# Kernel optimization log

Hardware: AMD Instinct MI355X
Metric: run time of the kernel (lower is better)

Reference implementation:

```python
import jax, jax.numpy as jnp
import numpy as np
import math

B, L, D, H = 4, 2048, 1024, 16
HD = D // H


def setup_inputs() -> dict:
    key = jax.random.key(0)
    k1, k2, k3 = jax.random.split(key, 3)
    x = jax.random.normal(k1, (B, L, D), dtype=jnp.float32)
    # Linear weights stored as [in, out] so y = x @ W (equivalent to torch x @ W.T)
    Wqkv = jax.random.normal(k2, (D, 3 * D), dtype=jnp.float32) * (1.0 / math.sqrt(D))
    Wproj = jax.random.normal(k3, (D, D), dtype=jnp.float32) * (1.0 / math.sqrt(D))
    attn_mask = jnp.tril(jnp.ones((L, L), dtype=bool))  # True = attend (causal)
    key_padding_mask = jnp.zeros((B, L), dtype=bool)     # True = padded (none here)
    return {"x": x, "Wqkv": Wqkv, "Wproj": Wproj,
            "attn_mask": attn_mask, "key_padding_mask": key_padding_mask}


def reference(x, Wqkv, Wproj, attn_mask, key_padding_mask):
    Bx, Lx, Dx = x.shape
    qkv = x @ Wqkv                              # [B, L, 3D]
    q, k, v = jnp.split(qkv, 3, axis=-1)
    def shape(t):
        return t.reshape(Bx, Lx, H, HD).transpose(0, 2, 1, 3)  # [B, H, L, hd]
    q, k, v = shape(q), shape(k), shape(v)
    att = jnp.einsum('bhqd,bhkd->bhqk', q, k) / math.sqrt(HD)  # [B, H, L, L]
    neg_inf = jnp.float32(-jnp.inf)
    att = jnp.where(attn_mask[None, None, :, :], att, neg_inf)
    att = jnp.where(key_padding_mask[:, None, None, :], neg_inf, att)
    att = jax.nn.softmax(att, axis=-1)
    y = jnp.einsum('bhqk,bhkd->bhqd', att, v)   # [B, H, L, hd]
    y = y.transpose(0, 2, 1, 3).reshape(Bx, Lx, Dx)
    return y @ Wproj
```

## Files before the change

kernel.cpp:

```cpp
#include <hip/hip_runtime.h>
#include <cstdint>
#include <cstddef>


typedef __attribute__((ext_vector_type(8))) __bf16 bf16x8;
typedef __attribute__((ext_vector_type(4))) __bf16 bf16x4;
typedef __attribute__((ext_vector_type(4))) float f32x4;
typedef __attribute__((ext_vector_type(16))) float f32x16;

__device__ __forceinline__ f32x4 mfma_bf16(bf16x8 a, bf16x8 b, f32x4 c) {
  return __builtin_amdgcn_mfma_f32_16x16x32_bf16(a, b, c, 0, 0, 0);
}

__device__ __forceinline__ f32x16 mfma32(bf16x8 a, bf16x8 b, f32x16 c) {
  return __builtin_amdgcn_mfma_f32_32x32x16_bf16(a, b, c, 0, 0, 0);
}

__device__ __forceinline__ unsigned cvtpk(float a, float b) {
  unsigned r;
  asm("v_cvt_pk_bf16_f32 %0, %1, %2" : "=v"(r) : "v"(a), "v"(b));
  return r;
}

__device__ __forceinline__ void async_copy16(const void* gsrc, void* ldsdst) {
  __builtin_amdgcn_global_load_lds(
      (const __attribute__((address_space(1))) void*)gsrc,
      (__attribute__((address_space(3))) void*)ldsdst, 16, 0, 0);
}

__global__ __launch_bounds__(256) void f32_to_bf16(
    const float* __restrict__ in, __bf16* __restrict__ out) {
  const size_t i = ((size_t)blockIdx.x * 256 + threadIdx.x) * 4;
  const float4 v = *(const float4*)&in[i];
  bf16x4 o = {(__bf16)v.x, (__bf16)v.y, (__bf16)v.z, (__bf16)v.w};
  *(bf16x4*)&out[i] = o;
}

__global__ __launch_bounds__(256) void transpose_f32_bf16(
    const float* __restrict__ in, __bf16* __restrict__ out, int R, int C) {
  __shared__ float tile[32][33];
  const int c0 = blockIdx.x * 32;
  const int r0 = blockIdx.y * 32;
  const int tx = threadIdx.x & 31;
  const int ty = threadIdx.x >> 5;
#pragma unroll
  for (int i = 0; i < 32; i += 8)
    tile[ty + i][tx] = in[(size_t)(r0 + ty + i) * C + c0 + tx];
  __syncthreads();
#pragma unroll
  for (int i = 0; i < 32; i += 8)
    out[(size_t)(c0 + ty + i) * R + r0 + tx] = (__bf16)tile[tx][ty + i];
}

#define GEMM128x128_CORE(Aptr, Bptr)                                         \
  const int srow32 = tid >> 3;                                    \
  const int schunk = ((tid & 7) ^ (srow32 & 7)) << 3;                        \
  const __bf16* aBase = &(Aptr)[(size_t)(m0 + srow32) * 1024 + schunk];      \
  const __bf16* bBase = &(Bptr)[(size_t)(n0 + srow32) * 1024 + schunk];      \
  auto stgTile = [&](int kt, int b2) {                                       \
    __bf16* dst = smem + b2 * 16384 + wave * 512;                            \
    _Pragma("unroll") for (int u = 0; u < 4; ++u)                            \
        async_copy16(aBase + (size_t)u * 32768 + kt * 64, dst + u * 2048);   \
    _Pragma("unroll") for (int u = 0; u < 4; ++u)                            \
        async_copy16(bBase + (size_t)u * 32768 + kt * 64,                    \
                     dst + 8192 + u * 2048);                                 \
  };                                                                         \
  const f32x4 zero = {0.f, 0.f, 0.f, 0.f};                                   \
  f32x4 acc[4][4];                                                           \
  _Pragma("unroll") for (int i = 0; i < 4; ++i)                              \
      _Pragma("unroll") for (int j = 0; j < 4; ++j) acc[i][j] = zero;        \
  stgTile(0, 0);                                                             \
  asm volatile("s_waitcnt vmcnt(0)" ::: "memory");                           \
  __builtin_amdgcn_s_barrier();                                              \
  for (int t = 0; t < 16; ++t) {                                             \
    const __bf16* As = smem + (t & 1) * 16384;                               \
    const __bf16* Bs = As + 8192;                                            \
    bf16x8 af[4][2], bfr[4][2];                                              \
    _Pragma("unroll") for (int mt = 0; mt < 4; ++mt)                         \
        _Pragma("unroll") for (int kk = 0; kk < 2; ++kk) af[mt][kk] =        \
            *(const bf16x8*)&As[(wr * 64 + mt * 16 + n16) * 64 +             \
                                (((kk * 4 + quad) ^ (n16 & 7)) << 3)];       \
    _Pragma("unroll") for (int nt = 0; nt < 4; ++nt)                         \
        _Pragma("unroll") for (int kk = 0; kk < 2; ++kk) bfr[nt][kk] =       \
            *(const bf16x8*)&Bs[(wc * 64 + nt * 16 + n16) * 64 +             \
                                (((kk * 4 + quad) ^ (n16 & 7)) << 3)];       \
    if (t < 15) stgTile(t + 1, (t + 1) & 1);                                 \
    __builtin_amdgcn_s_barrier();                                            \
    asm volatile("s_waitcnt lgkmcnt(0)" ::: "memory");                       \
    __builtin_amdgcn_sched_barrier(0);                                       \
    __builtin_amdgcn_s_setprio(1);                                           \
    _Pragma("unroll") for (int mt = 0; mt < 4; ++mt)                         \
        _Pragma("unroll") for (int nt = 0; nt < 4; ++nt)                     \
            _Pragma("unroll") for (int kk = 0; kk < 2; ++kk)                 \
                acc[mt][nt] = mfma_bf16(af[mt][kk], bfr[nt][kk],             \
                                        acc[mt][nt]);                        \
    __builtin_amdgcn_s_setprio(0);                                           \
    asm volatile("s_waitcnt vmcnt(0)" ::: "memory");                         \
    __builtin_amdgcn_s_barrier();                                            \
  }

__global__ __launch_bounds__(256, 2) void gemm_qkv(
    const __bf16* __restrict__ A, const __bf16* __restrict__ BT,
    __bf16* __restrict__ Q, __bf16* __restrict__ Kh, __bf16* __restrict__ VT) {
  extern __shared__ __bf16 smem[];
  const int wg = (blockIdx.x & 7) * 192 + (blockIdx.x >> 3);
  const int bm = wg / 24;
  const int bn = wg % 24;
  const int m0 = bm << 7;
  const int n0 = bn << 7;
  const int tid = threadIdx.x;
  const int wave = tid >> 6;
  const int lane = tid & 63;
  const int n16 = lane & 15;
  const int quad = lane >> 4;
  const int wr = wave >> 1;
  const int wc = wave & 1;

  GEMM128x128_CORE(A, BT)

  __bf16* tw = smem + wave * 2048;
  const int b = m0 >> 11;
  const int l0w = (m0 & 2047) + wr * 64;
  const int n = n0 + wc * 64;

  if (n < 2048) {
    const float QSCALE = 0.125f * 1.44269504089f;
    const bool isQ = (n < 1024);
    const int h = (n & 1023) >> 6;
    __bf16* dst = isQ ? Q : Kh;
    const size_t base = ((size_t)(b * 16 + h) * 2048) * 64;
#pragma unroll
    for (int pass = 0; pass < 2; ++pass) {
#pragma unroll
      for (int mt = 2 * pass; mt < 2 * pass + 2; ++mt) {
#pragma unroll
        for (int nt = 0; nt < 4; ++nt)
#pragma unroll
          for (int r = 0; r < 4; ++r) {
            const int hd = nt * 16 + n16;
            const int mm = (mt & 1) * 16 + quad * 4 + r;
            const float v = isQ ? acc[mt][nt][r] * QSCALE : acc[mt][nt][r];
            tw[mm * 64 + (((hd >> 3) ^ (mm & 7)) << 3) + (hd & 7)] =
                (__bf16)v;
          }
      }
#pragma unroll
      for (int i = 0; i < 4; ++i) {
        const int c = lane + 64 * i;
        const int row = c >> 3;
        const int hd0 = (c & 7) << 3;
        const int phys = (c & 7) ^ (row & 7);
        const bf16x8 v = *(const bf16x8*)&tw[row * 64 + phys * 8];
        *(bf16x8*)&dst[base + (size_t)(l0w + pass * 32 + row) * 64 + hd0] = v;
      }
    }
  } else {
    const int h = (n - 2048) >> 6;
    const size_t bhead = (size_t)(b * 16 + h);
#pragma unroll
    for (int pass = 0; pass < 2; ++pass) {
#pragma unroll
      for (int nt = 2 * pass; nt < 2 * pass + 2; ++nt) {
#pragma unroll
        for (int mt = 0; mt < 4; ++mt)
#pragma unroll
          for (int r = 0; r < 4; ++r) {
            const int hdp = (nt & 1) * 16 + n16;
            const int mm = mt * 16 + quad * 4 + r;
            const int phys = (mm >> 3) ^ (hdp & 7);
            tw[hdp * 64 + phys * 8 + (mm & 7)] = (__bf16)acc[mt][nt][r];
          }
      }
#pragma unroll
      for (int i = 0; i < 4; ++i) {
        const int c = lane + 64 * i;
        const int row = c >> 3;
        const int phys = (c & 7) ^ (row & 7);
        const bf16x8 v = *(const bf16x8*)&tw[row * 64 + phys * 8];
        *(bf16x8*)&VT[(bhead * 64 + pass * 32 + row) * 2048 + l0w +
                      (c & 7) * 8] = v;
      }
    }
  }
}

__global__ __launch_bounds__(256, 2) void gemm_bt_f32out(
    const __bf16* __restrict__ A, const __bf16* __restrict__ BT,
    float* __restrict__ C) {
  extern __shared__ __bf16 smem[];
  const int wg = (blockIdx.x & 7) * 64 + (blockIdx.x >> 3);
  const int bm = wg >> 3;
  const int bn = wg & 7;
  const int m0 = bm << 7;
  const int n0 = bn << 7;
  const int tid = threadIdx.x;
  const int wave = tid >> 6;
  const int lane = tid & 63;
  const int n16 = lane & 15;
  const int quad = lane >> 4;
  const int wr = wave >> 1;
  const int wc = wave & 1;

  GEMM128x128_CORE(A, BT)

#pragma unroll
  for (int mt = 0; mt < 4; ++mt) {
#pragma unroll
    for (int r = 0; r < 4; ++r) {
      const int m = m0 + wr * 64 + mt * 16 + quad * 4 + r;
#pragma unroll
      for (int nt = 0; nt < 4; ++nt) {
        const int nn = n0 + wc * 64 + nt * 16 + n16;
        C[(size_t)m * 1024 + nn] = acc[mt][nt][r];
      }
    }
  }
}

__global__ __launch_bounds__(256, 2) void flash_attn(
    const __bf16* __restrict__ Q, const __bf16* __restrict__ Kh,
    const __bf16* __restrict__ VT, __bf16* __restrict__ Y) {
  __shared__ __bf16 Ks[2][64 * 64];
  __shared__ __bf16 Vs[2][64 * 64];
  const int bh = blockIdx.x;
  const int p = blockIdx.y;
  const int tid = threadIdx.x;
  const int wave = tid >> 6;
  const int lane = tid & 63;
  const int lrow = lane & 31;
  const int hi = lane >> 5;
  const int lswz = lane & 7;
  const __bf16* Qb = Q + (size_t)bh * 2048 * 64;
  const __bf16* Kb = Kh + (size_t)bh * 2048 * 64;
  const __bf16* Vb = VT + (size_t)bh * 64 * 2048;
  const int b = bh >> 4;
  const int h = bh & 15;
  const f32x16 zero16 = {0.f, 0.f, 0.f, 0.f, 0.f, 0.f, 0.f, 0.f,
                         0.f, 0.f, 0.f, 0.f, 0.f, 0.f, 0.f, 0.f};

  const int srow = tid >> 3;
  const int sswz = ((tid & 7) ^ (srow & 7)) << 3;
  const size_t kg0 = (size_t)srow * 64 + sswz;
  const size_t kg1 = (size_t)(srow + 32) * 64 + sswz;
  const size_t vg0 = (size_t)srow * 2048 + sswz;
  const size_t vg1 = (size_t)(srow + 32) * 2048 + sswz;
  const int ldst0 = wave * 512;
  const int ldst1 = 2048 + wave * 512;

#pragma unroll
  for (int tt = 0; tt < 2; ++tt) {
    const int t = tt ? 15 - p : p;
    const int q0w = t * 128 + wave * 32;
    const int myq = q0w + lrow;

    bf16x8 qf[4];
#pragma unroll
    for (int i = 0; i < 4; ++i)
      qf[i] = *(const bf16x8*)&Qb[(size_t)myq * 64 + i * 16 + hi * 8];

    f32x16 o0 = zero16, o1 = zero16;
    float lsum = 0.f;
    const int nsteps = 2 * (t + 1);

    __syncthreads();
    async_copy16(&Kb[kg0], &Ks[0][ldst0]);
    async_copy16(&Kb[kg1], &Ks[0][ldst1]);
    async_copy16(&Vb[vg0], &Vs[0][ldst0]);
    async_copy16(&Vb[vg1], &Vs[0][ldst1]);

    for (int kt = 0; kt < nsteps; ++kt) {
      const int buf = kt & 1;
      const int c0 = kt << 6;
      __syncthreads();
      if (kt + 1 < nsteps) {
        const int nb = buf ^ 1;
        const int cn = c0 + 64;
        async_copy16(&Kb[kg0 + (size_t)cn * 64], &Ks[nb][ldst0]);
        async_copy16(&Kb[kg1 + (size_t)cn * 64], &Ks[nb][ldst1]);
        async_copy16(&Vb[vg0 + cn], &Vs[nb][ldst0]);
        async_copy16(&Vb[vg1 + cn], &Vs[nb][ldst1]);
      }
      if (c0 > q0w + 31) continue;

      const __bf16* ks = Ks[buf];
      const __bf16* vs = Vs[buf];

      f32x16 sc[2];
#pragma unroll
      for (int ch = 0; ch < 2; ++ch) {
        sc[ch] = zero16;
#pragma unroll
        for (int i = 0; i < 4; ++i) {
          const bf16x8 kf = *(const bf16x8*)&ks[(ch * 32 + lrow) * 64 +
                                                (((2 * i + hi) ^ lswz) << 3)];
          sc[ch] = mfma32(kf, qf[i], sc[ch]);
        }
      }
      if (c0 + 63 > q0w) {
#pragma unroll
        for (int ch = 0; ch < 2; ++ch)
#pragma unroll
          for (int r = 0; r < 16; ++r) {
            const int k = c0 + ch * 32 + (r & 3) + 8 * (r >> 2) + 4 * hi;
            float e = __builtin_amdgcn_exp2f(sc[ch][r]);
            e = (k <= myq) ? e : 0.f;
            sc[ch][r] = e;
            lsum += e;
          }
      } else {
#pragma unroll
        for (int ch = 0; ch < 2; ++ch)
#pragma unroll
          for (int r = 0; r < 16; ++r) {
            const float e = __builtin_amdgcn_exp2f(sc[ch][r]);
            sc[ch][r] = e;
            lsum += e;
          }
      }
#pragma unroll
      for (int ch = 0; ch < 2; ++ch) {
#pragma unroll
        for (int kc = 0; kc < 2; ++kc) {
          unsigned c01 = cvtpk(sc[ch][kc * 8 + 0], sc[ch][kc * 8 + 1]);
          unsigned c23 = cvtpk(sc[ch][kc * 8 + 2], sc[ch][kc * 8 + 3]);
          unsigned c45 = cvtpk(sc[ch][kc * 8 + 4], sc[ch][kc * 8 + 5]);
          unsigned c67 = cvtpk(sc[ch][kc * 8 + 6], sc[ch][kc * 8 + 7]);
          asm("v_permlane32_swap_b32 %0, %1" : "+v"(c01), "+v"(c45));
          asm("v_permlane32_swap_b32 %0, %1" : "+v"(c23), "+v"(c67));
          union {
            unsigned u[4];
            bf16x8 v;
          } pu;
          pu.u[0] = c01;
          pu.u[1] = c23;
          pu.u[2] = c45;
          pu.u[3] = c67;
          const int kch = ch * 4 + kc * 2 + hi;
          {
            const bf16x8 vf0 = *(const bf16x8*)&vs[(0 * 32 + lrow) * 64 +
                                                   ((kch ^ lswz) << 3)];
            o0 = mfma32(pu.v, vf0, o0);
            const bf16x8 vf1 = *(const bf16x8*)&vs[(1 * 32 + lrow) * 64 +
                                                   ((kch ^ lswz) << 3)];
            o1 = mfma32(pu.v, vf1, o1);
          }
        }
      }
    }

    lsum += __shfl_xor(lsum, 32);
    const float inv = 1.0f / lsum;
    float invr[16];
#pragma unroll
    for (int r = 0; r < 16; ++r)
      invr[r] = __shfl(inv, (r & 3) + 8 * (r >> 2) + 4 * hi);
#pragma unroll
    for (int r = 0; r < 16; ++r) {
      const int row = q0w + (r & 3) + 8 * (r >> 2) + 4 * hi;
      const size_t yb = (size_t)(b * 2048 + row) * 1024 + h * 64;
      Y[yb + lrow] = (__bf16)(o0[r] * invr[r]);
      Y[yb + 32 + lrow] = (__bf16)(o1[r] * invr[r]);
    }
  }
}

extern "C" void kernel_launch(void* const* d_in, const int* in_sizes, int n_in,
                              void* d_out, int out_size, void* d_ws,
                              size_t ws_size, hipStream_t stream) {
  const float* x = (const float*)d_in[0];
  const float* Wqkv = (const float*)d_in[1];
  const float* Wproj = (const float*)d_in[2];
  float* out = (float*)d_out;

  char* ws = (char*)d_ws;
  __bf16* xb = (__bf16*)ws;     ws += (size_t)8192 * 1024 * 2;
  __bf16* WqkvT = (__bf16*)ws;  ws += (size_t)3072 * 1024 * 2;
  __bf16* WprojT = (__bf16*)ws; ws += (size_t)1024 * 1024 * 2;
  __bf16* Qs = (__bf16*)ws;     ws += (size_t)64 * 2048 * 64 * 2;
  __bf16* Ks = (__bf16*)ws;     ws += (size_t)64 * 2048 * 64 * 2;
  __bf16* VTs = (__bf16*)ws;    ws += (size_t)64 * 64 * 2048 * 2;
  __bf16* attn = xb;

  static bool attrSet = false;
  if (!attrSet) {
    hipFuncSetAttribute((const void*)gemm_qkv,
                        hipFuncAttributeMaxDynamicSharedMemorySize, 65536);
    hipFuncSetAttribute((const void*)gemm_bt_f32out,
                        hipFuncAttributeMaxDynamicSharedMemorySize, 65536);
    attrSet = true;
  }

  f32_to_bf16<<<8192, 256, 0, stream>>>(x, xb);
  transpose_f32_bf16<<<dim3(96, 32), 256, 0, stream>>>(Wqkv, WqkvT, 1024, 3072);
  transpose_f32_bf16<<<dim3(32, 32), 256, 0, stream>>>(Wproj, WprojT, 1024, 1024);
  gemm_qkv<<<1536, 256, 65536, stream>>>(xb, WqkvT, Qs, Ks, VTs);
  flash_attn<<<dim3(64, 8), 256, 0, stream>>>(Qs, Ks, VTs, attn);
  gemm_bt_f32out<<<512, 256, 65536, stream>>>(attn, WprojT, out);
}
```

Measured before the change: 227.7 us.

## Merge prep kernels into one launch and stage 128-key KV tiles in attention

The three preprocessing launches (x cast plus two weight transposes) are merged into one kernel that dispatches on block index, which removes two launch gaps. The flash attention loop now stages 128 keys per double-buffered step, as two 64-key halves, so it needs half as many __syncthreads barriers per query tile. LDS use doubles to 64KB per block, which may limit how many blocks fit per CU. Causal skipping is kept per 64-key half.

Result: no change. 232.1 us (+1.9%).

```diff
diff --git a/kernel.cpp b/kernel.cpp
--- a/kernel.cpp
+++ b/kernel.cpp
@@ -28,19 +28,29 @@
       (__attribute__((address_space(3))) void*)ldsdst, 16, 0, 0);
 }
 
-__global__ __launch_bounds__(256) void f32_to_bf16(
-    const float* __restrict__ in, __bf16* __restrict__ out) {
-  const size_t i = ((size_t)blockIdx.x * 256 + threadIdx.x) * 4;
-  const float4 v = *(const float4*)&in[i];
-  bf16x4 o = {(__bf16)v.x, (__bf16)v.y, (__bf16)v.z, (__bf16)v.w};
-  *(bf16x4*)&out[i] = o;
-}
-
-__global__ __launch_bounds__(256) void transpose_f32_bf16(
-    const float* __restrict__ in, __bf16* __restrict__ out, int R, int C) {
+__global__ __launch_bounds__(256) void prep(
+    const float* __restrict__ x, __bf16* __restrict__ xb,
+    const float* __restrict__ Wqkv, __bf16* __restrict__ WqkvT,
+    const float* __restrict__ Wproj, __bf16* __restrict__ WprojT) {
+  const int bid = blockIdx.x;
+  if (bid < 8192) {
+    const size_t i = ((size_t)bid * 256 + threadIdx.x) * 4;
+    const float4 v = *(const float4*)&x[i];
+    bf16x4 o = {(__bf16)v.x, (__bf16)v.y, (__bf16)v.z, (__bf16)v.w};
+    *(bf16x4*)&xb[i] = o;
+    return;
+  }
   __shared__ float tile[32][33];
-  const int c0 = blockIdx.x * 32;
-  const int r0 = blockIdx.y * 32;
+  const float* in;
+  __bf16* out;
+  int idx, gx, R, C;
+  if (bid < 8192 + 3072) {
+    idx = bid - 8192; in = Wqkv; out = WqkvT; R = 1024; C = 3072; gx = 96;
+  } else {
+    idx = bid - 11264; in = Wproj; out = WprojT; R = 1024; C = 1024; gx = 32;
+  }
+  const int c0 = (idx % gx) * 32;
+  const int r0 = (idx / gx) * 32;
   const int tx = threadIdx.x & 31;
   const int ty = threadIdx.x >> 5;
 #pragma unroll
@@ -220,8 +230,8 @@
 __global__ __launch_bounds__(256, 2) void flash_attn(
     const __bf16* __restrict__ Q, const __bf16* __restrict__ Kh,
     const __bf16* __restrict__ VT, __bf16* __restrict__ Y) {
-  __shared__ __bf16 Ks[2][64 * 64];
-  __shared__ __bf16 Vs[2][64 * 64];
+  __shared__ __bf16 Ks[2][2][64 * 64];
+  __shared__ __bf16 Vs[2][2][64 * 64];
   const int bh = blockIdx.x;
   const int p = blockIdx.y;
   const int tid = threadIdx.x;
@@ -240,12 +250,22 @@
 
   const int srow = tid >> 3;
   const int sswz = ((tid & 7) ^ (srow & 7)) << 3;
-  const size_t kg0 = (size_t)srow * 64 + sswz;
-  const size_t kg1 = (size_t)(srow + 32) * 64 + sswz;
-  const size_t vg0 = (size_t)srow * 2048 + sswz;
-  const size_t vg1 = (size_t)(srow + 32) * 2048 + sswz;
-  const int ldst0 = wave * 512;
-  const int ldst1 = 2048 + wave * 512;
+  const int ldst = wave * 512;
+
+  auto stageKV = [&](int cn, int nb) {
+#pragma unroll
+    for (int hf = 0; hf < 2; ++hf)
+#pragma unroll
+      for (int rb = 0; rb < 2; ++rb)
+        async_copy16(&Kb[(size_t)(cn + hf * 64 + rb * 32 + srow) * 64 + sswz],
+                     &Ks[nb][hf][rb * 2048 + ldst]);
+#pragma unroll
+    for (int hf = 0; hf < 2; ++hf)
+#pragma unroll
+      for (int rb = 0; rb < 2; ++rb)
+        async_copy16(&Vb[(size_t)(rb * 32 + srow) * 2048 + cn + hf * 64 + sswz],
+                     &Vs[nb][hf][rb * 2048 + ldst]);
+  };
 
 #pragma unroll
   for (int tt = 0; tt < 2; ++tt) {
@@ -260,89 +280,83 @@
 
     f32x16 o0 = zero16, o1 = zero16;
     float lsum = 0.f;
-    const int nsteps = 2 * (t + 1);
+    const int nk = t + 1;
 
     __syncthreads();
-    async_copy16(&Kb[kg0], &Ks[0][ldst0]);
-    async_copy16(&Kb[kg1], &Ks[0][ldst1]);
-    async_copy16(&Vb[vg0], &Vs[0][ldst0]);
-    async_copy16(&Vb[vg1], &Vs[0][ldst1]);
-
-    for (int kt = 0; kt < nsteps; ++kt) {
+    stageKV(0, 0);
+
+    for (int kt = 0; kt < nk; ++kt) {
       const int buf = kt & 1;
-      const int c0 = kt << 6;
       __syncthreads();
-      if (kt + 1 < nsteps) {
-        const int nb = buf ^ 1;
-        const int cn = c0 + 64;
-        async_copy16(&Kb[kg0 + (size_t)cn * 64], &Ks[nb][ldst0]);
-        async_copy16(&Kb[kg1 + (size_t)cn * 64], &Ks[nb][ldst1]);
-        async_copy16(&Vb[vg0 + cn], &Vs[nb][ldst0]);
-        async_copy16(&Vb[vg1 + cn], &Vs[nb][ldst1]);
-      }
-      if (c0 > q0w + 31) continue;
-
-      const __bf16* ks = Ks[buf];
-      const __bf16* vs = Vs[buf];
-
-      f32x16 sc[2];
-#pragma unroll
-      for (int ch = 0; ch < 2; ++ch) {
-        sc[ch] = zero16;
-#pragma unroll
-        for (int i = 0; i < 4; ++i) {
-          const bf16x8 kf = *(const bf16x8*)&ks[(ch * 32 + lrow) * 64 +
-                                                (((2 * i + hi) ^ lswz) << 3)];
-          sc[ch] = mfma32(kf, qf[i], sc[ch]);
+      if (kt + 1 < nk) stageKV((kt + 1) << 7, buf ^ 1);
+
+#pragma unroll
+      for (int s = 0; s < 2; ++s) {
+        const int c0s = (kt << 7) + (s << 6);
+        if (c0s > q0w + 31) continue;
+        const __bf16* ks = Ks[buf][s];
+        const __bf16* vs = Vs[buf][s];
+
+        f32x16 sc[2];
+#pragma unroll
+        for (int ch = 0; ch < 2; ++ch) {
+          sc[ch] = zero16;
+#pragma unroll
+          for (int i = 0; i < 4; ++i) {
+            const bf16x8 kf = *(const bf16x8*)&ks[(ch * 32 + lrow) * 64 +
+                                                  (((2 * i + hi) ^ lswz)
+                                                   << 3)];
+            sc[ch] = mfma32(kf, qf[i], sc[ch]);
+          }
         }
-      }
-      if (c0 + 63 > q0w) {
-#pragma unroll
-        for (int ch = 0; ch < 2; ++ch)
-#pragma unroll
-          for (int r = 0; r < 16; ++r) {
-            const int k = c0 + ch * 32 + (r & 3) + 8 * (r >> 2) + 4 * hi;
-            float e = __builtin_amdgcn_exp2f(sc[ch][r]);
-            e = (k <= myq) ? e : 0.f;
-            sc[ch][r] = e;
-            lsum += e;
-          }
-      } else {
-#pragma unroll
-        for (int ch = 0; ch < 2; ++ch)
-#pragma unroll
-          for (int r = 0; r < 16; ++r) {
-            const float e = __builtin_amdgcn_exp2f(sc[ch][r]);
-            sc[ch][r] = e;
-            lsum += e;
-          }
-      }
-#pragma unroll
-      for (int ch = 0; ch < 2; ++ch) {
-#pragma unroll
-        for (int kc = 0; kc < 2; ++kc) {
-          unsigned c01 = cvtpk(sc[ch][kc * 8 + 0], sc[ch][kc * 8 + 1]);
-          unsigned c23 = cvtpk(sc[ch][kc * 8 + 2], sc[ch][kc * 8 + 3]);
-          unsigned c45 = cvtpk(sc[ch][kc * 8 + 4], sc[ch][kc * 8 + 5]);
-          unsigned c67 = cvtpk(sc[ch][kc * 8 + 6], sc[ch][kc * 8 + 7]);
-          asm("v_permlane32_swap_b32 %0, %1" : "+v"(c01), "+v"(c45));
-          asm("v_permlane32_swap_b32 %0, %1" : "+v"(c23), "+v"(c67));
-          union {
-            unsigned u[4];
-            bf16x8 v;
-          } pu;
-          pu.u[0] = c01;
-          pu.u[1] = c23;
-          pu.u[2] = c45;
-          pu.u[3] = c67;
-          const int kch = ch * 4 + kc * 2 + hi;
-          {
-            const bf16x8 vf0 = *(const bf16x8*)&vs[(0 * 32 + lrow) * 64 +
-                                                   ((kch ^ lswz) << 3)];
-            o0 = mfma32(pu.v, vf0, o0);
-            const bf16x8 vf1 = *(const bf16x8*)&vs[(1 * 32 + lrow) * 64 +
-                                                   ((kch ^ lswz) << 3)];
-            o1 = mfma32(pu.v, vf1, o1);
+        if (c0s + 63 > q0w) {
+#pragma unroll
+          for (int ch = 0; ch < 2; ++ch)
+#pragma unroll
+            for (int r = 0; r < 16; ++r) {
+              const int k = c0s + ch * 32 + (r & 3) + 8 * (r >> 2) + 4 * hi;
+              float e = __builtin_amdgcn_exp2f(sc[ch][r]);
+              e = (k <= myq) ? e : 0.f;
+              sc[ch][r] = e;
+              lsum += e;
+            }
+        } else {
+#pragma unroll
+          for (int ch = 0; ch < 2; ++ch)
+#pragma unroll
+            for (int r = 0; r < 16; ++r) {
+              const float e = __builtin_amdgcn_exp2f(sc[ch][r]);
+              sc[ch][r] = e;
+              lsum += e;
+            }
+        }
+#pragma unroll
+        for (int ch = 0; ch < 2; ++ch) {
+#pragma unroll
+          for (int kc = 0; kc < 2; ++kc) {
+            unsigned c01 = cvtpk(sc[ch][kc * 8 + 0], sc[ch][kc * 8 + 1]);
+            unsigned c23 = cvtpk(sc[ch][kc * 8 + 2], sc[ch][kc * 8 + 3]);
+            unsigned c45 = cvtpk(sc[ch][kc * 8 + 4], sc[ch][kc * 8 + 5]);
+            unsigned c67 = cvtpk(sc[ch][kc * 8 + 6], sc[ch][kc * 8 + 7]);
+            asm("v_permlane32_swap_b32 %0, %1" : "+v"(c01), "+v"(c45));
+            asm("v_permlane32_swap_b32 %0, %1" : "+v"(c23), "+v"(c67));
+            union {
+              unsigned u[4];
+              bf16x8 v;
+            } pu;
+            pu.u[0] = c01;
+            pu.u[1] = c23;
+            pu.u[2] = c45;
+            pu.u[3] = c67;
+            const int kch = ch * 4 + kc * 2 + hi;
+            {
+              const bf16x8 vf0 = *(const bf16x8*)&vs[(0 * 32 + lrow) * 64 +
+                                                     ((kch ^ lswz) << 3)];
+              o0 = mfma32(pu.v, vf0, o0);
+              const bf16x8 vf1 = *(const bf16x8*)&vs[(1 * 32 + lrow) * 64 +
+                                                     ((kch ^ lswz) << 3)];
+              o1 = mfma32(pu.v, vf1, o1);
+            }
           }
         }
       }
@@ -390,9 +404,7 @@
     attrSet = true;
   }
 
-  f32_to_bf16<<<8192, 256, 0, stream>>>(x, xb);
-  transpose_f32_bf16<<<dim3(96, 32), 256, 0, stream>>>(Wqkv, WqkvT, 1024, 3072);
-  transpose_f32_bf16<<<dim3(32, 32), 256, 0, stream>>>(Wproj, WprojT, 1024, 1024);
+  prep<<<12288, 256, 0, stream>>>(x, xb, Wqkv, WqkvT, Wproj, WprojT);
   gemm_qkv<<<1536, 256, 65536, stream>>>(xb, WqkvT, Qs, Ks, VTs);
   flash_attn<<<dim3(64, 8), 256, 0, stream>>>(Qs, Ks, VTs, attn);
   gemm_bt_f32out<<<512, 256, 65536, stream>>>(attn, WprojT, out);
```
